# Optimization experiments

Hardware: AMD Instinct MI355X
Metric: run time of the kernel (lower is better)

## Reference

```python
import jax, jax.numpy as jnp
import numpy as np
import math

DIM = 2048
NUM_HEADS = 16
HEAD_DIM = 128
SEQ = 2048
BATCH = 2
THETA = 10000.0


def _rope_freqs(seq_len, head_dim, theta=THETA):
    half = head_dim // 2
    inv = 1.0 / (theta ** (np.arange(0, half, dtype=np.float32) / half))
    t = np.arange(seq_len, dtype=np.float32)
    ang = np.outer(t, inv)  # [S, half]
    return jnp.asarray(np.cos(ang)), jnp.asarray(np.sin(ang))


def setup_inputs() -> dict:
    key = jax.random.key(0)
    ks = jax.random.split(key, 5)
    s = 1.0 / math.sqrt(DIM)
    cos, sin = _rope_freqs(SEQ, HEAD_DIM)
    return {
        "x": jax.random.normal(ks[0], (BATCH, SEQ, DIM), dtype=jnp.float32),
        "wq": jax.random.normal(ks[1], (DIM, NUM_HEADS * HEAD_DIM), dtype=jnp.float32) * s,
        "wk": jax.random.normal(ks[2], (DIM, NUM_HEADS * HEAD_DIM), dtype=jnp.float32) * s,
        "wv": jax.random.normal(ks[3], (DIM, NUM_HEADS * HEAD_DIM), dtype=jnp.float32) * s,
        "wo": jax.random.normal(ks[4], (NUM_HEADS * HEAD_DIM, DIM), dtype=jnp.float32) * s,
        "freqs_cos": cos,
        "freqs_sin": sin,
    }


def _apply_rope(x, cos, sin):
    # x: [B, S, H, Hd]; cos/sin: [S, Hd//2]
    B, S, H, Hd = x.shape
    xr = x.astype(jnp.float32).reshape(B, S, H, Hd // 2, 2)
    x0, x1 = xr[..., 0], xr[..., 1]
    c = cos[:S][None, :, None, :]
    sn = sin[:S][None, :, None, :]
    o0 = x0 * c - x1 * sn
    o1 = x0 * sn + x1 * c
    return jnp.stack([o0, o1], axis=-1).reshape(B, S, H, Hd)


def reference(x, wq, wk, wv, wo, freqs_cos, freqs_sin):
    B, S, D = x.shape
    H, Hd = NUM_HEADS, HEAD_DIM
    q = (x @ wq).reshape(B, S, H, Hd)
    k = (x @ wk).reshape(B, S, H, Hd)
    v = (x @ wv).reshape(B, S, H, Hd)
    q = _apply_rope(q, freqs_cos, freqs_sin)
    k = _apply_rope(k, freqs_cos, freqs_sin)
    # [B, H, S, S] causal attention scores
    scores = jnp.einsum("bqhd,bkhd->bhqk", q, k) / math.sqrt(Hd)
    causal = jnp.tril(jnp.ones((S, S), dtype=bool))
    scores = jnp.where(causal[None, None], scores, -jnp.inf)
    probs = jax.nn.softmax(scores.astype(jnp.float32), axis=-1)
    o = jnp.einsum("bhqk,bkhd->bqhd", probs, v).reshape(B, S, H * Hd)
    return o @ wo
```

## Files before the change

kernel.cpp:

```cpp
#include <hip/hip_runtime.h>
#include <hip/hip_bf16.h>

typedef __bf16 bf16;
typedef __attribute__((ext_vector_type(8))) __bf16 bf16x8;
typedef __attribute__((ext_vector_type(4))) __bf16 bf16x4;
typedef __attribute__((ext_vector_type(4))) float  f32x4;

typedef const void __attribute__((address_space(1)))* gas_t;
typedef void __attribute__((address_space(3)))* las_t;

__device__ __forceinline__ void gload16(const void* g, void* l) {
  __builtin_amdgcn_global_load_lds((gas_t)g, (las_t)l, 16, 0, 0);
}
__device__ __forceinline__ f32x4 mfma16(bf16x8 a, bf16x8 b, f32x4 c) {
  return __builtin_amdgcn_mfma_f32_16x16x32_bf16(a, b, c, 0, 0, 0);
}

constexpr int SEQL = 2048;
constexpr int DM   = 2048;
constexpr int HD   = 128;
constexpr int MR   = 4096;

__global__ __launch_bounds__(256) void cvt_x(const float* __restrict__ x,
                                             bf16* __restrict__ xb) {
  const size_t i = ((size_t)blockIdx.x * 256 + threadIdx.x) * 4;
  const f32x4 v = *reinterpret_cast<const f32x4*>(x + i);
  bf16x4 o;
  #pragma unroll
  for (int j = 0; j < 4; ++j) o[j] = (bf16)v[j];
  *reinterpret_cast<bf16x4*>(xb + i) = o;
}

__global__ __launch_bounds__(256) void transpose_w(
    const float* __restrict__ w0, const float* __restrict__ w1,
    const float* __restrict__ w2, const float* __restrict__ w3,
    bf16* __restrict__ wqkvt, bf16* __restrict__ wot) {
  const int z = blockIdx.z;
  const float* src = (z == 0) ? w0 : (z == 1) ? w1 : (z == 2) ? w2 : w3;
  bf16* dst = (z < 3) ? (wqkvt + (size_t)z * DM * DM) : wot;
  __shared__ float tile[32][33];
  const int tx = threadIdx.x, ty = threadIdx.y;
  const int x0 = blockIdx.x * 32, y0 = blockIdx.y * 32;
  #pragma unroll
  for (int i = 0; i < 4; ++i)
    tile[ty + 8 * i][tx] = src[(size_t)(y0 + ty + 8 * i) * DM + x0 + tx];
  __syncthreads();
  #pragma unroll
  for (int i = 0; i < 4; ++i)
    dst[(size_t)(x0 + ty + 8 * i) * DM + y0 + tx] = (bf16)tile[tx][ty + 8 * i];
}

__global__ __launch_bounds__(256) void rope_k(bf16* __restrict__ Q,
                                              bf16* __restrict__ Kk,
                                              const float* __restrict__ fc,
                                              const float* __restrict__ fs) {
  bf16* X = blockIdx.y ? Kk : Q;
  const size_t tid = (size_t)blockIdx.x * 256 + threadIdx.x;
  const size_t e0 = tid * 8;
  const int col = (int)(e0 & (DM - 1));
  const int row = (int)(e0 >> 11);
  const int s   = row & (SEQL - 1);
  const int p0  = (col & (HD - 1)) >> 1;
  bf16x8 v = *reinterpret_cast<bf16x8*>(X + e0);
  const f32x4 c  = *reinterpret_cast<const f32x4*>(fc + (size_t)s * 64 + p0);
  const f32x4 sn = *reinterpret_cast<const f32x4*>(fs + (size_t)s * 64 + p0);
  #pragma unroll
  for (int j = 0; j < 4; ++j) {
    const float x0 = (float)v[2 * j], x1 = (float)v[2 * j + 1];
    v[2 * j]     = (bf16)(x0 * c[j] - x1 * sn[j]);
    v[2 * j + 1] = (bf16)(x0 * sn[j] + x1 * c[j]);
  }
  *reinterpret_cast<bf16x8*>(X + e0) = v;
}

template <bool MULTI, bool OUTF32>
__global__ __launch_bounds__(256) void gemm_bt(
    const bf16* __restrict__ A, const bf16* __restrict__ Bt,
    bf16* __restrict__ Cb, float* __restrict__ Cf,
    const int M, const int N, const int K) {
  const int t = threadIdx.x;
  const int wid = t >> 6, lane = t & 63, lo = lane & 15, hi = lane >> 4;
  const int m0 = blockIdx.y * 128, n0 = blockIdx.x * 128;
  const bf16* Bt_ = Bt;
  bf16* Cb_ = Cb;
  if (MULTI) {
    const size_t z = blockIdx.z;
    Bt_ += z * (size_t)N * K;
    Cb_ += z * (size_t)M * N;
  }
  __shared__ bf16 As[128 * 32];
  __shared__ bf16 Bs[128 * 32];
  const int wr = wid >> 1, wc = wid & 1;
  const f32x4 zero4 = {0.f, 0.f, 0.f, 0.f};
  f32x4 acc[4][4];
  #pragma unroll
  for (int i = 0; i < 4; ++i)
    #pragma unroll
    for (int j = 0; j < 4; ++j) acc[i][j] = zero4;

  const int r_a = t >> 2;
  const int ul  = ((t & 3) ^ (r_a & 3)) * 8;
  const bf16* gA0 = A   + (size_t)(m0 + r_a) * K + ul;
  const bf16* gB0 = Bt_ + (size_t)(n0 + r_a) * K + ul;
  char* lA = (char*)As + wid * 1024;
  char* lB = (char*)Bs + wid * 1024;

  const int ru = (hi ^ (lo & 3)) * 8;

  for (int k0 = 0; k0 < K; k0 += 32) {
    gload16(gA0 + k0, lA);
    gload16(gA0 + (size_t)64 * K + k0, lA + 4096);
    gload16(gB0 + k0, lB);
    gload16(gB0 + (size_t)64 * K + k0, lB + 4096);
    __syncthreads();
    bf16x8 af[4], bb[4];
    #pragma unroll
    for (int i = 0; i < 4; ++i)
      af[i] = *reinterpret_cast<const bf16x8*>(As + (wr * 64 + i * 16 + lo) * 32 + ru);
    #pragma unroll
    for (int i = 0; i < 4; ++i)
      bb[i] = *reinterpret_cast<const bf16x8*>(Bs + (wc * 64 + i * 16 + lo) * 32 + ru);
    #pragma unroll
    for (int mi = 0; mi < 4; ++mi)
      #pragma unroll
      for (int ni = 0; ni < 4; ++ni)
        acc[mi][ni] = mfma16(af[mi], bb[ni], acc[mi][ni]);
    __syncthreads();
  }
  #pragma unroll
  for (int mi = 0; mi < 4; ++mi)
    #pragma unroll
    for (int ni = 0; ni < 4; ++ni)
      #pragma unroll
      for (int r = 0; r < 4; ++r) {
        const size_t row = m0 + wr * 64 + mi * 16 + hi * 4 + r;
        const size_t col = n0 + wc * 64 + ni * 16 + lo;
        if (OUTF32) Cf[row * N + col] = acc[mi][ni][r];
        else        Cb_[row * N + col] = (bf16)acc[mi][ni][r];
      }
}

__global__ __launch_bounds__(256) void flash_fwd(
    const bf16* __restrict__ Qg, const bf16* __restrict__ Kg,
    const bf16* __restrict__ Vg, bf16* __restrict__ Og) {
  const int t = threadIdx.x;
  const int wid = t >> 6, lane = t & 63, lo = lane & 15, hi = lane >> 4;
  const int h  = blockIdx.y;
  const int b  = blockIdx.z;

  __shared__ bf16 Ks[64 * 128];
  __shared__ bf16 Vt[128 * 64];
  __shared__ bf16 Ps[4][16 * 64];

  const size_t hoff = (size_t)b * SEQL * DM + (size_t)h * HD;
  const float SCALE_LOG2 = 0.12751743f;

  const int krow = t >> 4;
  const int kul  = ((t & 15) ^ krow) * 8;
  const int vd0  = (t & 31) * 4;
  const int vg   = t >> 5;
  char* myP = (char*)(Ps[wid]);
  const f32x4 zero4 = {0.f, 0.f, 0.f, 0.f};

  #pragma unroll 1
  for (int pass = 0; pass < 2; ++pass) {
    const int q0 = (pass ? (31 - (int)blockIdx.x) : (int)blockIdx.x) * 64;

    bf16x8 qf[4];
    {
      const bf16* qrow = Qg + hoff + (size_t)(q0 + wid * 16 + lo) * DM;
      #pragma unroll
      for (int kc = 0; kc < 4; ++kc)
        qf[kc] = *reinterpret_cast<const bf16x8*>(qrow + kc * 32 + hi * 8);
    }

    f32x4 acc[8];
    #pragma unroll
    for (int i = 0; i < 8; ++i) acc[i] = zero4;
    float m_run = -1e30f, l_run = 0.f;

    const int ntiles = q0 / 64 + 1;
    #pragma unroll 1
    for (int it = 0; it < ntiles; ++it) {
      const int kv0 = it * 64;
      {
        const bf16* gK = Kg + hoff + (size_t)(kv0 + krow) * DM + kul;
        char* lK = (char*)Ks + wid * 1024;
        #pragma unroll
        for (int j = 0; j < 4; ++j)
          gload16(gK + (size_t)j * 16 * DM, lK + j * 4096);
      }
      {
        const bf16* gV = Vg + hoff + (size_t)kv0 * DM + vd0;
        bf16x4 ld[8];
        #pragma unroll
        for (int e = 0; e < 8; ++e)
          ld[e] = *reinterpret_cast<const bf16x4*>(gV + (size_t)(vg * 8 + e) * DM);
        #pragma unroll
        for (int c = 0; c < 4; ++c) {
          const int d = vd0 + c;
          const int sw = (d ^ (d >> 3)) & 7;
          bf16x8 pk;
          #pragma unroll
          for (int e = 0; e < 8; ++e) pk[e] = ld[e][c];
          *reinterpret_cast<bf16x8*>(Vt + d * 64 + ((vg ^ sw) * 8)) = pk;
        }
      }
      __syncthreads();

      f32x4 s[4];
      #pragma unroll
      for (int nf = 0; nf < 4; ++nf) s[nf] = zero4;
      #pragma unroll
      for (int nf = 0; nf < 4; ++nf) {
        const bf16* krp = Ks + (nf * 16 + lo) * 128;
        #pragma unroll
        for (int kc = 0; kc < 4; ++kc) {
          const bf16x8 kb = *reinterpret_cast<const bf16x8*>(krp + (((kc * 4 + hi) ^ lo) * 8));
          s[nf] = mfma16(kb, qf[kc], s[nf]);
        }
      }
      const bool boundary = (kv0 == q0);
      #pragma unroll
      for (int nf = 0; nf < 4; ++nf)
        #pragma unroll
        for (int r = 0; r < 4; ++r) {
          float v = s[nf][r] * SCALE_LOG2;
          if (boundary && (nf * 16 + hi * 4 + r > wid * 16 + lo)) v = -1e30f;
          s[nf][r] = v;
        }
      float pmax = -1e30f;
      #pragma unroll
      for (int nf = 0; nf < 4; ++nf)
        #pragma unroll
        for (int r = 0; r < 4; ++r) pmax = fmaxf(pmax, s[nf][r]);
      pmax = fmaxf(pmax, __shfl_xor(pmax, 16, 64));
      pmax = fmaxf(pmax, __shfl_xor(pmax, 32, 64));
      float mnew = m_run;
      if (!__all(pmax <= m_run)) {
        mnew = fmaxf(m_run, pmax);
        const float fctr = exp2f(m_run - mnew);
        m_run = mnew;
        l_run *= fctr;
        float fa[4];
        #pragma unroll
        for (int r = 0; r < 4; ++r) fa[r] = __shfl(fctr, hi * 4 + r, 64);
        #pragma unroll
        for (int i = 0; i < 8; ++i)
          #pragma unroll
          for (int r = 0; r < 4; ++r) acc[i][r] *= fa[r];
      }
      float sum = 0.f;
      #pragma unroll
      for (int nf = 0; nf < 4; ++nf)
        #pragma unroll
        for (int r = 0; r < 4; ++r) {
          const float p = exp2f(s[nf][r] - mnew);
          s[nf][r] = p;
          sum += p;
        }
      sum += __shfl_xor(sum, 16, 64);
      sum += __shfl_xor(sum, 32, 64);
      l_run += sum;
      #pragma unroll
      for (int nf = 0; nf < 4; ++nf) {
        bf16x4 w;
        #pragma unroll
        for (int r = 0; r < 4; ++r) w[r] = (bf16)s[nf][r];
        *reinterpret_cast<bf16x4*>(myP + lo * 128 +
            (((nf * 2 + (hi >> 1)) ^ (lo & 7)) * 16) + (hi & 1) * 8) = w;
      }
      bf16x8 pa[2];
      #pragma unroll
      for (int kc = 0; kc < 2; ++kc)
        pa[kc] = *reinterpret_cast<const bf16x8*>(myP + lo * 128 +
            (((kc * 4 + hi) ^ (lo & 7)) * 16));
      #pragma unroll
      for (int nf = 0; nf < 8; ++nf) {
        const int d = nf * 16 + lo;
        const int sw = (d ^ (d >> 3)) & 7;
        const bf16* vrp = Vt + d * 64;
        #pragma unroll
        for (int kc = 0; kc < 2; ++kc) {
          const bf16x8 bv = *reinterpret_cast<const bf16x8*>(vrp + (((kc * 4 + hi) ^ sw) * 8));
          acc[nf] = mfma16(pa[kc], bv, acc[nf]);
        }
      }
      __syncthreads();
    }

    const float linv = 1.f / l_run;
    float la[4];
    #pragma unroll
    for (int r = 0; r < 4; ++r) la[r] = __shfl(linv, hi * 4 + r, 64);
    #pragma unroll
    for (int nf = 0; nf < 8; ++nf)
      #pragma unroll
      for (int r = 0; r < 4; ++r) {
        const size_t row = q0 + wid * 16 + hi * 4 + r;
        Og[hoff + row * DM + nf * 16 + lo] = (bf16)(acc[nf][r] * la[r]);
      }
  }
}

extern "C" void kernel_launch(void* const* d_in, const int* in_sizes, int n_in,
                              void* d_out, int out_size, void* d_ws, size_t ws_size,
                              hipStream_t stream) {
  const float* x  = (const float*)d_in[0];
  const float* wq = (const float*)d_in[1];
  const float* wk = (const float*)d_in[2];
  const float* wv = (const float*)d_in[3];
  const float* wo = (const float*)d_in[4];
  const float* fc = (const float*)d_in[5];
  const float* fs = (const float*)d_in[6];
  float* out = (float*)d_out;

  char* ws = (char*)d_ws;
  bf16* xb    = (bf16*)ws;
  bf16* wqkvt = (bf16*)(ws + (16ull << 20));
  bf16* wot   = (bf16*)(ws + (40ull << 20));
  bf16* qkv   = (bf16*)(ws + (48ull << 20));
  bf16* Qb = qkv;
  bf16* Kb = qkv + (size_t)MR * DM;
  bf16* Vb = qkv + 2 * (size_t)MR * DM;

  cvt_x<<<8192, 256, 0, stream>>>(x, xb);
  transpose_w<<<dim3(64, 64, 4), dim3(32, 8), 0, stream>>>(wq, wk, wv, wo, wqkvt, wot);
  gemm_bt<true, false><<<dim3(16, 32, 3), 256, 0, stream>>>(xb, wqkvt, qkv, nullptr, MR, DM, DM);
  rope_k<<<dim3(4096, 2), 256, 0, stream>>>(Qb, Kb, fc, fs);
  flash_fwd<<<dim3(16, 16, 2), 256, 0, stream>>>(Qb, Kb, Vb, xb );
  gemm_bt<false, true><<<dim3(16, 32), 256, 0, stream>>>(xb, wot, nullptr, out, MR, DM, DM);
}
```

Baseline: 437.9 us.

## Replace QKV GEMM with 256x256-tile, 8-wave, double-buffered pipelined kernel

The fused QKV projection GEMM moves to a new kernel that uses 256x256 output tiles, 512 threads (8 waves), and a 64-wide K step. It double-buffers A and B tiles in 128KB of LDS and issues the global-to-LDS loads for the next tiles in quarter-phases interleaved with MFMA work, using explicit vmcnt waits, barriers and s_setprio. The aim is to hide global load latency and raise arithmetic intensity compared with the old 128x128 tile kernel, which synchronised twice per K step. It relies on hand-written waitcnt accounting and large LDS use, which limits occupancy. The output projection stays on the old kernel, now specialised to f32 output.

After: 423.8 us. 3.2% less time.

```diff
diff --git a/kernel.cpp b/kernel.cpp
--- a/kernel.cpp
+++ b/kernel.cpp
@@ -73,21 +73,121 @@
   *reinterpret_cast<bf16x8*>(X + e0) = v;
 }
 
-template <bool MULTI, bool OUTF32>
-__global__ __launch_bounds__(256) void gemm_bt(
+#define GPH(Q, STAGE, TAIL)                                                    \
+  {                                                                            \
+    const char* ap = aB + ((Q) * 32 + lo) * 128;                               \
+    const bf16x8 a00 = *(const bf16x8*)(ap + su0);                             \
+    const bf16x8 a01 = *(const bf16x8*)(ap + su1);                             \
+    const bf16x8 a10 = *(const bf16x8*)(ap + 2048 + su0);                      \
+    const bf16x8 a11 = *(const bf16x8*)(ap + 2048 + su1);                      \
+    STAGE                                                                      \
+    __builtin_amdgcn_s_barrier();                                              \
+    asm volatile("s_waitcnt lgkmcnt(0)" ::: "memory");                         \
+    __builtin_amdgcn_s_setprio(1);                                             \
+    _Pragma("unroll")                                                          \
+    for (int nf = 0; nf < 4; ++nf) {                                           \
+      acc[2 * (Q)][nf]     = mfma16(a00, bfr[nf][0], acc[2 * (Q)][nf]);        \
+      acc[2 * (Q)][nf]     = mfma16(a01, bfr[nf][1], acc[2 * (Q)][nf]);        \
+      acc[2 * (Q) + 1][nf] = mfma16(a10, bfr[nf][0], acc[2 * (Q) + 1][nf]);    \
+      acc[2 * (Q) + 1][nf] = mfma16(a11, bfr[nf][1], acc[2 * (Q) + 1][nf]);    \
+    }                                                                          \
+    __builtin_amdgcn_s_setprio(0);                                             \
+    TAIL                                                                       \
+    __builtin_amdgcn_s_barrier();                                              \
+    asm volatile("" ::: "memory");                                             \
+  }
+
+template <bool MULTI>
+__global__ __launch_bounds__(512, 2) void gemm8(
     const bf16* __restrict__ A, const bf16* __restrict__ Bt,
-    bf16* __restrict__ Cb, float* __restrict__ Cf,
-    const int M, const int N, const int K) {
+    bf16* __restrict__ Cb, const int M, const int N, const int K) {
+  __shared__ __attribute__((aligned(16))) char lds[131072];
+  const int t = threadIdx.x;
+  const int wid = t >> 6, lane = t & 63, lo = lane & 15, hi = lane >> 4;
+  const int wm = wid >> 2, wn = wid & 3;
+
+  const int bid = blockIdx.x;
+  const int nx = bid & 7;
+  const int my = MULTI ? ((bid >> 3) & 15) : (bid >> 3);
+  const int z  = MULTI ? (bid >> 7) : 0;
+  const int m0 = my * 256, n0 = nx * 256;
+  const bf16* Bt_ = Bt + (MULTI ? (size_t)z * N * K : 0);
+  bf16* Cb_ = Cb + (MULTI ? (size_t)z * M * N : 0);
+
+  const int urow  = (wid << 3) + (lane >> 3);
+  const int uunit = (lane & 7) ^ ((lane >> 3) & 7);
+  const bf16* gA = A   + (size_t)(m0 + urow) * K + uunit * 8;
+  const bf16* gB = Bt_ + (size_t)(n0 + urow) * K + uunit * 8;
+  char* lw = lds + wid * 1024;
+
+  const int NT = K >> 6;
+
+  auto stg = [&](const bf16* gbase, int buf, int op, int h, int kt) {
+    const bf16* g = gbase + (size_t)(h * 128) * K + kt * 64;
+    char* l = lw + (((buf << 1) | op) * 2 + h) * 16384;
+    gload16(g, l);
+    gload16(g + (size_t)64 * K, l + 8192);
+  };
+  auto stB0 = [&](int kt2) { stg(gB, kt2 & 1, 1, 0, kt2); };
+  auto stB1 = [&](int kt2) { stg(gB, kt2 & 1, 1, 1, kt2); };
+  auto stA0 = [&](int kt2) { stg(gA, kt2 & 1, 0, 0, kt2); };
+  auto stA1 = [&](int kt2) { stg(gA, kt2 & 1, 0, 1, kt2); };
+
+  f32x4 acc[8][4];
+  #pragma unroll
+  for (int i = 0; i < 8; ++i)
+    #pragma unroll
+    for (int j = 0; j < 4; ++j) acc[i][j] = (f32x4){0.f, 0.f, 0.f, 0.f};
+
+  const int su0 = (hi ^ (lo & 7)) * 16;
+  const int su1 = ((4 + hi) ^ (lo & 7)) * 16;
+
+  stB0(0); stB1(0); stA0(0); stA1(0);
+  stB0(1); stB1(1); stA0(1);
+  asm volatile("s_waitcnt vmcnt(6)" ::: "memory");
+  __builtin_amdgcn_s_barrier();
+  asm volatile("" ::: "memory");
+
+  #pragma unroll 1
+  for (int kt = 0; kt < NT; ++kt) {
+    const int bufc = kt & 1;
+    const char* aB = lds + ((bufc * 2 + 0) * 2 + wm) * 16384;
+    const char* bB = lds + ((bufc * 2 + 1) * 2 + (wn >> 1)) * 16384;
+    bf16x8 bfr[4][2];
+    {
+      const char* bp = bB + ((wn & 1) * 64 + lo) * 128;
+      #pragma unroll
+      for (int nf = 0; nf < 4; ++nf) {
+        bfr[nf][0] = *(const bf16x8*)(bp + nf * 2048 + su0);
+        bfr[nf][1] = *(const bf16x8*)(bp + nf * 2048 + su1);
+      }
+    }
+    GPH(0, if (kt + 1 < NT) stA1(kt + 1);, )
+    GPH(1, if (kt + 2 < NT) stB0(kt + 2);, )
+    GPH(2, if (kt + 2 < NT) stB1(kt + 2);, )
+    GPH(3, if (kt + 2 < NT) stA0(kt + 2);,
+        if (kt + 2 < NT) { asm volatile("s_waitcnt vmcnt(6)" ::: "memory"); }
+        else             { asm volatile("s_waitcnt vmcnt(0)" ::: "memory"); })
+  }
+
+  #pragma unroll
+  for (int mf = 0; mf < 8; ++mf)
+    #pragma unroll
+    for (int nf = 0; nf < 4; ++nf)
+      #pragma unroll
+      for (int r = 0; r < 4; ++r) {
+        const size_t row = m0 + wm * 128 + mf * 16 + hi * 4 + r;
+        const size_t col = n0 + wn * 64 + nf * 16 + lo;
+        Cb_[row * N + col] = (bf16)acc[mf][nf][r];
+      }
+}
+
+__global__ __launch_bounds__(256) void gemm_bt_f32(
+    const bf16* __restrict__ A, const bf16* __restrict__ Bt,
+    float* __restrict__ Cf, const int M, const int N, const int K) {
   const int t = threadIdx.x;
   const int wid = t >> 6, lane = t & 63, lo = lane & 15, hi = lane >> 4;
   const int m0 = blockIdx.y * 128, n0 = blockIdx.x * 128;
-  const bf16* Bt_ = Bt;
-  bf16* Cb_ = Cb;
-  if (MULTI) {
-    const size_t z = blockIdx.z;
-    Bt_ += z * (size_t)N * K;
-    Cb_ += z * (size_t)M * N;
-  }
   __shared__ bf16 As[128 * 32];
   __shared__ bf16 Bs[128 * 32];
   const int wr = wid >> 1, wc = wid & 1;
@@ -100,8 +200,8 @@
 
   const int r_a = t >> 2;
   const int ul  = ((t & 3) ^ (r_a & 3)) * 8;
-  const bf16* gA0 = A   + (size_t)(m0 + r_a) * K + ul;
-  const bf16* gB0 = Bt_ + (size_t)(n0 + r_a) * K + ul;
+  const bf16* gA0 = A  + (size_t)(m0 + r_a) * K + ul;
+  const bf16* gB0 = Bt + (size_t)(n0 + r_a) * K + ul;
   char* lA = (char*)As + wid * 1024;
   char* lB = (char*)Bs + wid * 1024;
 
@@ -135,8 +235,7 @@
       for (int r = 0; r < 4; ++r) {
         const size_t row = m0 + wr * 64 + mi * 16 + hi * 4 + r;
         const size_t col = n0 + wc * 64 + ni * 16 + lo;
-        if (OUTF32) Cf[row * N + col] = acc[mi][ni][r];
-        else        Cb_[row * N + col] = (bf16)acc[mi][ni][r];
+        Cf[row * N + col] = acc[mi][ni][r];
       }
 }
 
@@ -326,8 +425,8 @@
 
   cvt_x<<<8192, 256, 0, stream>>>(x, xb);
   transpose_w<<<dim3(64, 64, 4), dim3(32, 8), 0, stream>>>(wq, wk, wv, wo, wqkvt, wot);
-  gemm_bt<true, false><<<dim3(16, 32, 3), 256, 0, stream>>>(xb, wqkvt, qkv, nullptr, MR, DM, DM);
+  gemm8<true><<<384, 512, 0, stream>>>(xb, wqkvt, qkv, MR, DM, DM);
   rope_k<<<dim3(4096, 2), 256, 0, stream>>>(Qb, Kb, fc, fs);
   flash_fwd<<<dim3(16, 16, 2), 256, 0, stream>>>(Qb, Kb, Vb, xb );
-  gemm_bt<false, true><<<dim3(16, 32), 256, 0, stream>>>(xb, wot, nullptr, out, MR, DM, DM);
-}
+  gemm_bt_f32<<<dim3(16, 32), 256, 0, stream>>>(xb, wot, out, MR, DM, DM);
+}
```
